# Performance work log

Hardware: AMD Instinct MI355X
Metric: run time of the kernel (lower is better)

## Reference

```python
import jax, jax.numpy as jnp
import numpy as np

NUM_FRAMES = 8
NUM_CLASSES = 40
INNER_TH = 0.5
MIN_WH = 0.05
SUPPRESS = 1e9


def _xyxy_to_cxcywh(b):
    x1, y1, x2, y2 = b[..., 0], b[..., 1], b[..., 2], b[..., 3]
    return jnp.stack([(x1 + x2) * 0.5, (y1 + y2) * 0.5, x2 - x1, y2 - y1], -1)


def setup_inputs() -> dict:
    key = jax.random.key(0)
    k1, k2, k3, k4, k5 = jax.random.split(key, 5)
    B, N, T = 4, 20, NUM_FRAMES
    H = W = 160
    # valid xyxy boxes: centers in [0.1,0.9], wh in [0.02,0.3]
    c = jax.random.uniform(k1, (B, N, T, 2), minval=0.1, maxval=0.9)
    wh = jax.random.uniform(k2, (B, N, T, 2), minval=0.02, maxval=0.3)
    gt_boxes = jnp.concatenate([c - wh / 2, c + wh / 2], -1).astype(jnp.float32)
    gt_labels = jax.random.randint(k3, (B, N), 0, NUM_CLASSES)
    ids = jax.random.randint(k4, (B, N, T), 0, 100)
    drop = jax.random.bernoulli(k5, 0.1, (B, N, T))
    gt_ids = jnp.where(drop, -1, ids)  # -1 => instance absent in that frame
    ys, xs = jnp.meshgrid(jnp.arange(H), jnp.arange(W), indexing='ij')
    ref_points = jnp.stack([(xs.reshape(-1) + 0.5) / W, (ys.reshape(-1) + 0.5) / H], -1).astype(jnp.float32)
    spatial_shapes = jnp.array([H, W], dtype=jnp.int32)
    return dict(gt_labels=gt_labels, gt_boxes=gt_boxes, gt_ids=gt_ids,
                ref_points=ref_points, spatial_shapes=spatial_shapes)


def _match_frame(dist_t, ids_t, labels, valid):
    # dist_t [N,P], ids_t [N], labels [N], valid [N]; sequential suppression over n
    N, P = dist_t.shape
    arangeP = jnp.arange(P)
    arangeC = jnp.arange(NUM_CLASSES)

    def step(carry, n):
        d_all, ml, md, mi = carry
        d = d_all[n]                                   # [P]
        act = valid[n] & (ids_t[n] != -1)
        inner = d < INNER_TH
        # if no inner point, claim just the single closest point
        pos = jnp.where(inner.any(), inner, arangeP == jnp.argmin(d)) & act
        lab = labels[n]
        score = 1.0 - 2.0 * jnp.clip(d, 0.0, INNER_TH)
        ml = jnp.where(pos, lab, ml)
        md = jnp.where(pos[:, None] & (arangeC == lab)[None, :], score[:, None], md)
        mi = jnp.where(pos, ids_t[n], mi)
        d_all = jnp.where(pos[None, :], SUPPRESS, d_all)  # suppress claimed points for all gts
        return (d_all, ml, md, mi), None

    init = (dist_t,
            jnp.full((P,), -1, jnp.int32),
            jnp.zeros((P, NUM_CLASSES), dist_t.dtype),
            jnp.full((P,), -1, jnp.int32))
    (_, ml, md, mi), _ = jax.lax.scan(step, init, jnp.arange(N))
    return ml, md, mi


def reference(gt_labels, gt_boxes, gt_ids, ref_points, spatial_shapes):
    B, N, T, _ = gt_boxes.shape
    boxes_c = _xyxy_to_cxcywh(gt_boxes)                 # [B,N,T,4]
    area = (boxes_c[..., 2] * boxes_c[..., 3]).mean(-1)  # [B,N] mean area over frames
    order = jnp.argsort(area, axis=1)                   # process small instances first
    boxes_c = jnp.take_along_axis(boxes_c, order[:, :, None, None], axis=1)
    labels = jnp.take_along_axis(gt_labels.astype(jnp.int32), order, axis=1)
    ids = jnp.take_along_axis(gt_ids.astype(jnp.int32), order[:, :, None], axis=1)
    valid = (boxes_c[..., 2:] > 0.0).all(-1).any(-1) & (labels >= 0)  # [B,N]
    # normalized center distance: [B,N,T,P]
    diff = (boxes_c[..., None, :2] - ref_points[None, None, None, :, :]) / jnp.clip(boxes_c[..., None, 2:], MIN_WH)
    dist = jnp.sum(diff ** 2, -1)
    f = jax.vmap(jax.vmap(_match_frame, in_axes=(1, 1, None, None)), in_axes=(0, 0, 0, 0))
    ml, md, mi = f(dist, ids, labels, valid)            # [B,T,P], [B,T,P,C], [B,T,P]
    return ml, md, mi
```

## Files before the change

### kernel.cpp

```cpp
#include <hip/hip_runtime.h>

#define BB   4
#define NGT  20
#define TT   8
#define PP   25600
#define CC   40
#define TPB  1024
#define SUPP 1e9f
#define INNER_TH 0.5f
#define FILLB 224
#define NONEC 63u
#define FBF   64u

__device__ inline unsigned long long shfl_down_u64(unsigned long long v, int off) {
    unsigned lo = (unsigned)v, hi = (unsigned)(v >> 32);
    lo = __shfl_down(lo, off, 64);
    hi = __shfl_down(hi, off, 64);
    return ((unsigned long long)hi << 32) | (unsigned long long)lo;
}

__device__ inline float4 make_geo(const float* __restrict__ gt_boxes, int b, int n, int t) {
    const float* bx = gt_boxes + ((size_t)(b * NGT + n) * TT + t) * 4;
    float x1 = bx[0], y1 = bx[1], x2 = bx[2], y2 = bx[3];
    float4 g;
    g.x = __fmul_rn(__fadd_rn(x1, x2), 0.5f);
    g.y = __fmul_rn(__fadd_rn(y1, y2), 0.5f);
    g.z = fmaxf(__fsub_rn(x2, x1), 0.05f);
    g.w = fmaxf(__fsub_rn(y2, y1), 0.05f);
    return g;
}

__device__ inline float point_dist(int px, int py, float4 g) {
    float rxv = __fdiv_rn((float)px + 0.5f, 160.0f);
    float ryv = __fdiv_rn((float)py + 0.5f, 160.0f);
    float dx = __fdiv_rn(__fsub_rn(g.x, rxv), g.z);
    float dy = __fdiv_rn(__fsub_rn(g.y, ryv), g.w);
    return __fadd_rn(__fmul_rn(dx, dx), __fmul_rn(dy, dy));
}

__global__ __launch_bounds__(TPB) void match_fill_kernel(
        const int*   __restrict__ gt_labels,
        const float* __restrict__ gt_boxes,
        const int*   __restrict__ gt_ids,
        unsigned char* __restrict__ cand_ws,
        int4*          __restrict__ meta_ws,
        unsigned char* __restrict__ supp_ws,
        uint4*         __restrict__ md4) {
    if (blockIdx.x >= BB * TT) {
        const int MD4 = BB * TT * PP * CC / 4;
        const int stride = FILLB * TPB;
        uint4 z = make_uint4(0u, 0u, 0u, 0u);
        for (int i = (blockIdx.x - BB * TT) * TPB + (int)threadIdx.x; i < MD4; i += stride)
            md4[i] = z;
        return;
    }

    int bt = blockIdx.x;
    int b  = bt >> 3;
    int t  = bt & 7;
    int tid  = threadIdx.x;
    int lane = tid & 63;

    __shared__ unsigned      s_cand[PP];
    __shared__ unsigned char s_candb[PP];
    __shared__ unsigned      s_mask[160 * 5];
    __shared__ float  s_dxx[NGT * 160];
    __shared__ float  s_dyy[NGT * 160];
    __shared__ float  s_area[NGT];
    __shared__ int    s_valid[NGT];
    __shared__ int    s_order[NGT];
    __shared__ float4 s_geo[NGT];
    __shared__ int4   s_meta[NGT];
    __shared__ int    s_actlist[NGT];
    __shared__ int    s_actcnt;
    __shared__ int    s_count[NGT];
    __shared__ unsigned long long s_wave[TPB / 64];
    __shared__ unsigned s_suppmd;

    {
        uint4 ini = make_uint4(NONEC * 0x01010101u, NONEC * 0x01010101u,
                               NONEC * 0x01010101u, NONEC * 0x01010101u);
        uint4 iniw = make_uint4(NONEC, NONEC, NONEC, NONEC);
        (void)ini;
        for (int i = tid; i < PP / 4; i += TPB) ((uint4*)s_cand)[i] = iniw;
    }
    if (tid < NGT) {
        const float* bx = gt_boxes + (size_t)(b * NGT + tid) * TT * 4;
        float a[TT];
        int anyPos = 0;
        for (int f = 0; f < TT; f++) {
            float w = __fsub_rn(bx[f * 4 + 2], bx[f * 4 + 0]);
            float h = __fsub_rn(bx[f * 4 + 3], bx[f * 4 + 1]);
            a[f] = __fmul_rn(w, h);
            anyPos |= (w > 0.0f && h > 0.0f) ? 1 : 0;
        }
        float s = __fadd_rn(__fadd_rn(__fadd_rn(a[0], a[1]), __fadd_rn(a[2], a[3])),
                            __fadd_rn(__fadd_rn(a[4], a[5]), __fadd_rn(a[6], a[7])));
        s_area[tid]  = __fmul_rn(s, 0.125f);
        s_valid[tid] = (anyPos && gt_labels[b * NGT + tid] >= 0) ? 1 : 0;
        s_count[tid] = 0;
    }
    if (tid == 0) s_suppmd = 255u;
    __syncthreads();

    if (tid < NGT) {
        float an = s_area[tid];
        int r = 0;
        for (int m2 = 0; m2 < NGT; m2++) {
            float am = s_area[m2];
            r += (am < an || (am == an && m2 < tid)) ? 1 : 0;
        }
        s_order[r] = tid;
    }
    __syncthreads();

    if (tid < NGT) {
        int n   = s_order[tid];
        int src = b * NGT + n;
        s_geo[tid] = make_geo(gt_boxes, b, n, t);
        int id = gt_ids[src * TT + t];
        int4 mm;
        mm.x = gt_labels[src];
        mm.y = id;
        mm.z = (s_valid[n] && id != -1) ? 1 : 0;
        mm.w = n;
        s_meta[tid] = mm;
    }
    __syncthreads();
    if (tid == 0) {
        int c = 0;
        for (int k = 0; k < NGT; k++)
            if (s_meta[k].z) s_actlist[c++] = k;
        s_actcnt = c;
    }

    for (int i = tid; i < NGT * 320; i += TPB) {
        int slot = i / 320;
        int w    = i - slot * 320;
        float4 g = s_geo[slot];
        if (w < 160) {
            float rxv = __fdiv_rn((float)w + 0.5f, 160.0f);
            float dx  = __fdiv_rn(__fsub_rn(g.x, rxv), g.z);
            s_dxx[slot * 160 + w] = __fmul_rn(dx, dx);
        } else {
            int py = w - 160;
            float ryv = __fdiv_rn((float)py + 0.5f, 160.0f);
            float dy  = __fdiv_rn(__fsub_rn(g.y, ryv), g.w);
            s_dyy[slot * 160 + py] = __fmul_rn(dy, dy);
        }
    }
    __syncthreads();
    int actcnt = s_actcnt;

    for (int jj = 0; jj < actcnt; jj++) {
        int slot = s_actlist[jj];
        float4 g = s_geo[slot];
        const float* dxx = s_dxx + slot * 160;
        const float* dyy = s_dyy + slot * 160;
        float ex = __fmul_rn(g.z, 0.70711f);
        float ey = __fmul_rn(g.w, 0.70711f);
        int x0 = max(0,   (int)floorf((g.x - ex) * 160.0f - 0.5f) - 1);
        int x1 = min(159, (int)ceilf ((g.x + ex) * 160.0f - 0.5f) + 1);
        int y0 = max(0,   (int)floorf((g.y - ey) * 160.0f - 0.5f) - 1);
        int y1 = min(159, (int)ceilf ((g.y + ey) * 160.0f - 0.5f) + 1);
        int rw = x1 - x0 + 1;
        int M  = rw * (y1 - y0 + 1);
        int r  = tid / rw;
        int c  = tid - r * rw;
        int dr = TPB / rw;
        int dc = TPB - dr * rw;
        for (int i = tid; i < M; i += TPB) {
            int px = x0 + c;
            int py = y0 + r;
            float d = __fadd_rn(dxx[px], dyy[py]);
            if (d < INNER_TH) atomicMin(&s_cand[py * 160 + px], (unsigned)slot);
            c += dc; r += dr;
            if (c >= rw) { c -= rw; r++; }
        }
    }
    __syncthreads();

    {
        unsigned lcnt = 0;
        for (int i = tid; i < PP; i += TPB) {
            unsigned cc = s_cand[i];
            s_candb[i] = (unsigned char)cc;
            for (int k = 0; k < NGT; k++) {
                unsigned long long bl = __ballot(cc == (unsigned)k);
                if (lane == k) lcnt += (unsigned)__popcll(bl);
            }
        }
        if (lane < NGT) atomicAdd(&s_count[lane], (int)lcnt);
    }
    __syncthreads();

    for (int jj = 0; jj < actcnt; jj++) {
        int slot = s_actlist[jj];
        if (s_count[slot] != 0) continue;

        int4 m  = s_meta[slot];
        float4 g = s_geo[slot];
        const float* dxx = s_dxx + slot * 160;
        const float* dyy = s_dyy + slot * 160;

        for (int w = tid; w < 160 * 5; w += TPB) {
            const unsigned* cw = ((const unsigned*)s_candb) + (w << 3);
            unsigned mb = 0u;
#pragma unroll
            for (int q = 0; q < 8; q++) {
                unsigned v = cw[q];
                mb |= (((v        & 63u) < (unsigned)slot) ? 1u : 0u) << (q * 4 + 0);
                mb |= ((((v >> 8)  & 63u) < (unsigned)slot) ? 1u : 0u) << (q * 4 + 1);
                mb |= ((((v >> 16) & 63u) < (unsigned)slot) ? 1u : 0u) << (q * 4 + 2);
                mb |= ((((v >> 24) & 63u) < (unsigned)slot) ? 1u : 0u) << (q * 4 + 3);
            }
            s_mask[w] = mb;
        }
        __syncthreads();

        unsigned long long key = ~0ULL;
        if (tid < 160) {
            int y = tid;
            unsigned um[5];
#pragma unroll
            for (int w = 0; w < 5; w++) um[w] = ~s_mask[y * 5 + w];
            unsigned anyu = um[0] | um[1] | um[2] | um[3] | um[4];
            if (!anyu) {
                if (y == 0)
                    key = ((unsigned long long)__float_as_uint(SUPP) << 32);
            } else {
                float dyyv = dyy[y];
                int xs = (int)floorf(__fsub_rn(__fmul_rn(g.x, 160.0f), 0.5f));
                xs = min(max(xs, -2), 161);
                float bd = 2e9f;
                int   bx = -1;
#pragma unroll
                for (int k2 = 0; k2 < 2; k2++) {
                    int x = xs + k2;
                    if (x >= 0 && x <= 159 && ((um[x >> 5] >> (x & 31)) & 1u)) {
                        float d2 = __fadd_rn(dxx[x], dyyv);
                        if (d2 < bd || (d2 == bd && x < bx)) { bd = d2; bx = x; }
                    }
                }
                {
                    int xq = min(xs - 1, 159);
                    int xL = -1;
                    if (xq >= 0) {
                        int w = xq >> 5;
                        unsigned mm = um[w] & (0xffffffffu >> (31 - (xq & 31)));
                        while (true) {
                            if (mm) { xL = (w << 5) + (31 - __clz(mm)); break; }
                            if (--w < 0) break;
                            mm = um[w];
                        }
                    }
                    if (xL >= 0) {
                        float dL = __fadd_rn(dxx[xL], dyyv);
                        while (xL > 0) {
                            int xq2 = xL - 1;
                            int w = xq2 >> 5;
                            unsigned mm = um[w] & (0xffffffffu >> (31 - (xq2 & 31)));
                            int x2 = -1;
                            while (true) {
                                if (mm) { x2 = (w << 5) + (31 - __clz(mm)); break; }
                                if (--w < 0) break;
                                mm = um[w];
                            }
                            if (x2 < 0) break;
                            if (__fadd_rn(dxx[x2], dyyv) != dL) break;
                            xL = x2;
                        }
                        if (dL < bd || (dL == bd && xL < bx)) { bd = dL; bx = xL; }
                    }
                }
                {
                    int xq = max(xs + 2, 0);
                    int xR = -1;
                    if (xq <= 159) {
                        int w = xq >> 5;
                        unsigned mm = um[w] & (0xffffffffu << (xq & 31));
                        while (true) {
                            if (mm) { xR = (w << 5) + (__ffs(mm) - 1); break; }
                            if (++w > 4) break;
                            mm = um[w];
                        }
                    }
                    if (xR >= 0) {
                        float dR = __fadd_rn(dxx[xR], dyyv);
                        if (dR < bd || (dR == bd && xR < bx)) { bd = dR; bx = xR; }
                    }
                }
                if (bx >= 0) {
                    int p = y * 160 + bx;
                    key = ((unsigned long long)__float_as_uint(bd) << 32) |
                          (unsigned long long)(unsigned)p;
                }
            }
        }
        unsigned long long v = key;
        for (int off = 32; off > 0; off >>= 1) {
            unsigned long long o = shfl_down_u64(v, off);
            v = (o < v) ? o : v;
        }
        if (lane == 0) s_wave[tid >> 6] = v;
        __syncthreads();
        if (tid == 0) {
            unsigned long long gmin = s_wave[0];
            for (int w = 1; w < TPB / 64; w++)
                gmin = (s_wave[w] < gmin) ? s_wave[w] : gmin;
            float minv = __uint_as_float((unsigned)(gmin >> 32));
            int minp = (int)(unsigned)(gmin & 0xffffffffu);
            if (minv < SUPP) {
                unsigned old = s_candb[minp];
                if (old != NONEC) s_count[old]--;
                s_candb[minp] = (unsigned char)((unsigned)slot | FBF);
            } else {
                unsigned old = s_candb[0];
                unsigned curmd = (old & FBF) ? s_suppmd :
                                 ((old != NONEC) ? (unsigned)old : 255u);
                if (curmd != 255u && s_meta[curmd & 63u].x == m.x) curmd = 255u;
                s_suppmd = curmd;
                s_candb[0] = (unsigned char)((unsigned)slot | FBF);
            }
        }
        __syncthreads();
    }

    for (int i = tid; i < PP / 16; i += TPB)
        ((uint4*)(cand_ws + (size_t)bt * PP))[i] = ((const uint4*)s_candb)[i];
    if (tid < NGT) {
        int4 mm = s_meta[tid];
        meta_ws[bt * NGT + tid] = make_int4(mm.x, mm.y, mm.w, 0);
    }
    if (tid == 0) supp_ws[bt] = (unsigned char)s_suppmd;
}

__global__ __launch_bounds__(256) void scatter_kernel(
        const unsigned char* __restrict__ cand_ws,
        const int4*          __restrict__ meta_ws,
        const unsigned char* __restrict__ supp_ws,
        const float*         __restrict__ gt_boxes,
        float* __restrict__ out) {
    const int ML = BB * TT * PP;
    const size_t MD = (size_t)BB * TT * PP * CC;
    const int MDOFF4 = (int)((ML + MD) / 4);
    int f4 = blockIdx.x * 256 + threadIdx.x;
    unsigned cw = ((const unsigned*)cand_ws)[f4];
    int bt = f4 / (PP / 4);
    const int4* mt = meta_ws + bt * NGT;

    float4 vml, vmi;
#pragma unroll
    for (int k = 0; k < 4; k++) {
        unsigned c = (cw >> (8 * k)) & 255u;
        float ml, mi;
        if (c == NONEC) { ml = -1.0f; mi = -1.0f; }
        else {
            int4 mr = mt[c & 63u];
            ml = (float)mr.x;
            mi = (float)mr.y;
        }
        ((float*)&vml)[k] = ml;
        ((float*)&vmi)[k] = mi;
    }
    ((float4*)out)[f4] = vml;
    ((float4*)out)[MDOFF4 + f4] = vmi;

    int pt0 = f4 << 2;
#pragma unroll
    for (int k = 0; k < 4; k++) {
        unsigned c = (cw >> (8 * k)) & 255u;
        if (c != NONEC && !(c & FBF)) {
            int pt = pt0 + k;
            int p  = pt - bt * PP;
            int4 mr = mt[c];
            float4 g = make_geo(gt_boxes, bt >> 3, mr.z, bt & 7);
            int py = p / 160;
            int px = p - py * 160;
            float d = point_dist(px, py, g);
            out[ML + (size_t)pt * CC + mr.x] = __fsub_rn(1.0f, __fmul_rn(2.0f, d));
        }
    }
    if (f4 % (PP / 4) == 0) {
        unsigned sm = supp_ws[bt];
        if (sm != 255u) {
            int4 mr = mt[sm & 63u];
            float4 g = make_geo(gt_boxes, bt >> 3, mr.z, bt & 7);
            float d = point_dist(0, 0, g);
            out[ML + (size_t)bt * PP * CC + mr.x] = __fsub_rn(1.0f, __fmul_rn(2.0f, d));
        }
    }
}

extern "C" void kernel_launch(void* const* d_in, const int* in_sizes, int n_in,
                              void* d_out, int out_size, void* d_ws, size_t ws_size,
                              hipStream_t stream) {
    const int*   gt_labels = (const int*)d_in[0];
    const float* gt_boxes  = (const float*)d_in[1];
    const int*   gt_ids    = (const int*)d_in[2];

    unsigned char* cand_ws = (unsigned char*)d_ws;
    int4*          meta_ws = (int4*)((char*)d_ws + BB * TT * PP);
    unsigned char* supp_ws = (unsigned char*)d_ws + BB * TT * PP
                             + BB * TT * NGT * (int)sizeof(int4);
    float*         outf    = (float*)d_out;

    match_fill_kernel<<<BB * TT + FILLB, TPB, 0, stream>>>(
        gt_labels, gt_boxes, gt_ids, cand_ws, meta_ws, supp_ws,
        (uint4*)(outf + BB * TT * PP));

    scatter_kernel<<<(BB * TT * PP / 4) / 256, 256, 0, stream>>>(
        cand_ws, meta_ws, supp_ws, gt_boxes, outf);
}
```

Measured before the change: 167.9 us.

## Split inner-point rasterization into per-GT bitmask kernel and resolve by first-claimer

Moves the per-(batch,frame,gt) inner-point rasterization out of the 32-block match kernel into a new 512-block kernel that writes per-GT bitmasks to workspace, alongside the output zero-fill. The finish kernel then loads these masks and resolves ownership per 32-pixel word with a first-claimer bitwise scan instead of shared-memory atomicMin over 25600 slots. This spreads the serial per-GT loop across many more blocks and removes atomic contention. In exchange it adds an extra kernel launch, about 2 MB of workspace traffic, and each settle block recomputes the area sort for every unit it handles.

Result: slower. 186.7 us (+11.2%).

```diff
diff --git a/kernel.cpp b/kernel.cpp
--- a/kernel.cpp
+++ b/kernel.cpp
@@ -6,11 +6,13 @@
 #define PP   25600
 #define CC   40
 #define TPB  1024
+#define ATPB 256
+#define ABLK 512
 #define SUPP 1e9f
 #define INNER_TH 0.5f
-#define FILLB 224
 #define NONEC 63u
 #define FBF   64u
+#define NW    800
 
 __device__ inline unsigned long long shfl_down_u64(unsigned long long v, int off) {
     unsigned lo = (unsigned)v, hi = (unsigned)(v >> 32);
@@ -38,30 +40,125 @@
     return __fadd_rn(__fmul_rn(dx, dx), __fmul_rn(dy, dy));
 }
 
-__global__ __launch_bounds__(TPB) void match_fill_kernel(
+__global__ __launch_bounds__(ATPB) void settle_fill_kernel(
         const int*   __restrict__ gt_labels,
         const float* __restrict__ gt_boxes,
         const int*   __restrict__ gt_ids,
+        unsigned*    __restrict__ mask_ws,
+        uint4*       __restrict__ md4) {
+    __shared__ float    s_area[NGT];
+    __shared__ int      s_valid[NGT];
+    __shared__ int      s_order[NGT];
+    __shared__ float    s_dxx[160];
+    __shared__ float    s_dyy[160];
+    __shared__ unsigned s_m[NW];
+    int tid = threadIdx.x;
+
+    for (int u = blockIdx.x; u < BB * TT * NGT; u += ABLK) {
+        int bt = u / NGT;
+        int s  = u - bt * NGT;
+        int b  = bt >> 3;
+        int t  = bt & 7;
+        __syncthreads();
+
+        if (tid < NGT) {
+            const float* bx = gt_boxes + (size_t)(b * NGT + tid) * TT * 4;
+            float a[TT];
+            int anyPos = 0;
+            for (int f = 0; f < TT; f++) {
+                float w = __fsub_rn(bx[f * 4 + 2], bx[f * 4 + 0]);
+                float h = __fsub_rn(bx[f * 4 + 3], bx[f * 4 + 1]);
+                a[f] = __fmul_rn(w, h);
+                anyPos |= (w > 0.0f && h > 0.0f) ? 1 : 0;
+            }
+            float sum = __fadd_rn(__fadd_rn(__fadd_rn(a[0], a[1]), __fadd_rn(a[2], a[3])),
+                                  __fadd_rn(__fadd_rn(a[4], a[5]), __fadd_rn(a[6], a[7])));
+            s_area[tid]  = __fmul_rn(sum, 0.125f);
+            s_valid[tid] = (anyPos && gt_labels[b * NGT + tid] >= 0) ? 1 : 0;
+        }
+        __syncthreads();
+        if (tid < NGT) {
+            float an = s_area[tid];
+            int r = 0;
+            for (int m2 = 0; m2 < NGT; m2++) {
+                float am = s_area[m2];
+                r += (am < an || (am == an && m2 < tid)) ? 1 : 0;
+            }
+            s_order[r] = tid;
+        }
+        __syncthreads();
+
+        int n  = s_order[s];
+        int id = gt_ids[(b * NGT + n) * TT + t];
+        int active = (s_valid[n] && id != -1) ? 1 : 0;
+        if (!active) continue;
+
+        float4 g = make_geo(gt_boxes, b, n, t);
+        for (int w = tid; w < 320; w += ATPB) {
+            if (w < 160) {
+                float rxv = __fdiv_rn((float)w + 0.5f, 160.0f);
+                float dx  = __fdiv_rn(__fsub_rn(g.x, rxv), g.z);
+                s_dxx[w] = __fmul_rn(dx, dx);
+            } else {
+                int py = w - 160;
+                float ryv = __fdiv_rn((float)py + 0.5f, 160.0f);
+                float dy  = __fdiv_rn(__fsub_rn(g.y, ryv), g.w);
+                s_dyy[py] = __fmul_rn(dy, dy);
+            }
+        }
+        for (int i = tid; i < NW; i += ATPB) s_m[i] = 0u;
+        __syncthreads();
+
+        float ex = __fmul_rn(g.z, 0.70711f);
+        float ey = __fmul_rn(g.w, 0.70711f);
+        int x0 = max(0,   (int)floorf((g.x - ex) * 160.0f - 0.5f) - 1);
+        int x1 = min(159, (int)ceilf ((g.x + ex) * 160.0f - 0.5f) + 1);
+        int y0 = max(0,   (int)floorf((g.y - ey) * 160.0f - 0.5f) - 1);
+        int y1 = min(159, (int)ceilf ((g.y + ey) * 160.0f - 0.5f) + 1);
+        int rw = x1 - x0 + 1;
+        int M  = rw * (y1 - y0 + 1);
+        {
+            int r  = tid / rw;
+            int c  = tid - r * rw;
+            int dr = ATPB / rw;
+            int dc = ATPB - dr * rw;
+            for (int i = tid; i < M; i += ATPB) {
+                int px = x0 + c;
+                int py = y0 + r;
+                float d = __fadd_rn(s_dxx[px], s_dyy[py]);
+                if (d < INNER_TH) {
+                    int p = py * 160 + px;
+                    atomicOr(&s_m[p >> 5], 1u << (p & 31));
+                }
+                c += dc; r += dr;
+                if (c >= rw) { c -= rw; r++; }
+            }
+        }
+        __syncthreads();
+        unsigned* gm = mask_ws + ((size_t)bt * NGT + s) * NW;
+        for (int i = tid; i < NW; i += ATPB) gm[i] = s_m[i];
+    }
+
+    const int MD4 = BB * TT * PP * CC / 4;
+    uint4 z = make_uint4(0u, 0u, 0u, 0u);
+    for (int i = blockIdx.x * ATPB + tid; i < MD4; i += ABLK * ATPB) md4[i] = z;
+}
+
+__global__ __launch_bounds__(TPB) void finish_kernel(
+        const int*   __restrict__ gt_labels,
+        const float* __restrict__ gt_boxes,
+        const int*   __restrict__ gt_ids,
+        const unsigned* __restrict__ mask_ws,
         unsigned char* __restrict__ cand_ws,
         int4*          __restrict__ meta_ws,
-        unsigned char* __restrict__ supp_ws,
-        uint4*         __restrict__ md4) {
-    if (blockIdx.x >= BB * TT) {
-        const int MD4 = BB * TT * PP * CC / 4;
-        const int stride = FILLB * TPB;
-        uint4 z = make_uint4(0u, 0u, 0u, 0u);
-        for (int i = (blockIdx.x - BB * TT) * TPB + (int)threadIdx.x; i < MD4; i += stride)
-            md4[i] = z;
-        return;
-    }
-
+        unsigned char* __restrict__ supp_ws) {
     int bt = blockIdx.x;
     int b  = bt >> 3;
     int t  = bt & 7;
     int tid  = threadIdx.x;
     int lane = tid & 63;
 
-    __shared__ unsigned      s_cand[PP];
+    __shared__ unsigned      s_gmask[NGT * NW];
     __shared__ unsigned char s_candb[PP];
     __shared__ unsigned      s_mask[160 * 5];
     __shared__ float  s_dxx[NGT * 160];
@@ -77,13 +174,6 @@
     __shared__ unsigned long long s_wave[TPB / 64];
     __shared__ unsigned s_suppmd;
 
-    {
-        uint4 ini = make_uint4(NONEC * 0x01010101u, NONEC * 0x01010101u,
-                               NONEC * 0x01010101u, NONEC * 0x01010101u);
-        uint4 iniw = make_uint4(NONEC, NONEC, NONEC, NONEC);
-        (void)ini;
-        for (int i = tid; i < PP / 4; i += TPB) ((uint4*)s_cand)[i] = iniw;
-    }
     if (tid < NGT) {
         const float* bx = gt_boxes + (size_t)(b * NGT + tid) * TT * 4;
         float a[TT];
@@ -102,7 +192,6 @@
     }
     if (tid == 0) s_suppmd = 255u;
     __syncthreads();
-
     if (tid < NGT) {
         float an = s_area[tid];
         int r = 0;
@@ -113,7 +202,6 @@
         s_order[r] = tid;
     }
     __syncthreads();
-
     if (tid < NGT) {
         int n   = s_order[tid];
         int src = b * NGT + n;
@@ -133,7 +221,6 @@
             if (s_meta[k].z) s_actlist[c++] = k;
         s_actcnt = c;
     }
-
     for (int i = tid; i < NGT * 320; i += TPB) {
         int slot = i / 320;
         int w    = i - slot * 320;
@@ -152,39 +239,46 @@
     __syncthreads();
     int actcnt = s_actcnt;
 
-    for (int jj = 0; jj < actcnt; jj++) {
-        int slot = s_actlist[jj];
-        float4 g = s_geo[slot];
-        const float* dxx = s_dxx + slot * 160;
-        const float* dyy = s_dyy + slot * 160;
-        float ex = __fmul_rn(g.z, 0.70711f);
-        float ey = __fmul_rn(g.w, 0.70711f);
-        int x0 = max(0,   (int)floorf((g.x - ex) * 160.0f - 0.5f) - 1);
-        int x1 = min(159, (int)ceilf ((g.x + ex) * 160.0f - 0.5f) + 1);
-        int y0 = max(0,   (int)floorf((g.y - ey) * 160.0f - 0.5f) - 1);
-        int y1 = min(159, (int)ceilf ((g.y + ey) * 160.0f - 0.5f) + 1);
-        int rw = x1 - x0 + 1;
-        int M  = rw * (y1 - y0 + 1);
-        int r  = tid / rw;
-        int c  = tid - r * rw;
-        int dr = TPB / rw;
-        int dc = TPB - dr * rw;
-        for (int i = tid; i < M; i += TPB) {
-            int px = x0 + c;
-            int py = y0 + r;
-            float d = __fadd_rn(dxx[px], dyy[py]);
-            if (d < INNER_TH) atomicMin(&s_cand[py * 160 + px], (unsigned)slot);
-            c += dc; r += dr;
-            if (c >= rw) { c -= rw; r++; }
-        }
+    for (int idx = tid; idx < actcnt * NW; idx += TPB) {
+        int jj = idx / NW;
+        int i  = idx - jj * NW;
+        s_gmask[jj * NW + i] =
+            mask_ws[((size_t)bt * NGT + s_actlist[jj]) * NW + i];
+    }
+    __syncthreads();
+
+    if (tid < NW) {
+        int wi = tid;
+        unsigned acc[8];
+#pragma unroll
+        for (int q = 0; q < 8; q++) acc[q] = NONEC * 0x01010101u;
+        unsigned done = 0u;
+        for (int jj = 0; jj < actcnt; jj++) {
+            unsigned mw = s_gmask[jj * NW + wi] & ~done;
+            if (mw) {
+                unsigned sb = (unsigned)s_actlist[jj] * 0x01010101u;
+#pragma unroll
+                for (int q = 0; q < 8; q++) {
+                    unsigned nib = (mw >> (q * 4)) & 0xFu;
+                    unsigned sel = ((nib & 1u) ? 0x000000FFu : 0u) |
+                                   ((nib & 2u) ? 0x0000FF00u : 0u) |
+                                   ((nib & 4u) ? 0x00FF0000u : 0u) |
+                                   ((nib & 8u) ? 0xFF000000u : 0u);
+                    acc[q] = (acc[q] & ~sel) | (sb & sel);
+                }
+                done |= mw;
+            }
+        }
+#pragma unroll
+        for (int q = 0; q < 8; q++)
+            ((unsigned*)s_candb)[wi * 8 + q] = acc[q];
     }
     __syncthreads();
 
     {
         unsigned lcnt = 0;
         for (int i = tid; i < PP; i += TPB) {
-            unsigned cc = s_cand[i];
-            s_candb[i] = (unsigned char)cc;
+            unsigned cc = s_candb[i];
             for (int k = 0; k < NGT; k++) {
                 unsigned long long bl = __ballot(cc == (unsigned)k);
                 if (lane == k) lcnt += (unsigned)__popcll(bl);
@@ -400,14 +494,16 @@
     const int*   gt_ids    = (const int*)d_in[2];
 
     unsigned char* cand_ws = (unsigned char*)d_ws;
-    int4*          meta_ws = (int4*)((char*)d_ws + BB * TT * PP);
-    unsigned char* supp_ws = (unsigned char*)d_ws + BB * TT * PP
-                             + BB * TT * NGT * (int)sizeof(int4);
+    unsigned*      mask_ws = (unsigned*)((char*)d_ws + 819200);
+    int4*          meta_ws = (int4*)((char*)d_ws + 819200 + 2048000);
+    unsigned char* supp_ws = (unsigned char*)d_ws + 819200 + 2048000 + 10240;
     float*         outf    = (float*)d_out;
 
-    match_fill_kernel<<<BB * TT + FILLB, TPB, 0, stream>>>(
-        gt_labels, gt_boxes, gt_ids, cand_ws, meta_ws, supp_ws,
-        (uint4*)(outf + BB * TT * PP));
+    settle_fill_kernel<<<ABLK, ATPB, 0, stream>>>(
+        gt_labels, gt_boxes, gt_ids, mask_ws, (uint4*)(outf + BB * TT * PP));
+
+    finish_kernel<<<BB * TT, TPB, 0, stream>>>(
+        gt_labels, gt_boxes, gt_ids, mask_ws, cand_ws, meta_ws, supp_ws);
 
     scatter_kernel<<<(BB * TT * PP / 4) / 256, 256, 0, stream>>>(
         cand_ws, meta_ws, supp_ws, gt_boxes, outf);
```
